# Kernel tuning notes

Measured on AMD Instinct MI355X. Metric: run time of the kernel, lower is better.

## Reference

```python
import jax, jax.numpy as jnp
import numpy as np

RESOLUTION = 2 ** 8  # 256
N_POINTS = 2 ** 21


def setup_inputs() -> dict:
    key = jax.random.key(0)
    k1, k2 = jax.random.split(key)
    inp = jax.random.uniform(k1, (N_POINTS, 3), dtype=jnp.float32)
    grid = jax.random.normal(k2, (RESOLUTION, RESOLUTION, RESOLUTION, 3), dtype=jnp.float32) * 0.01
    return {"input": inp, "feature_params": grid}


def reference(input, feature_params):
    R = feature_params.shape[0]
    scaled = input * (R - 1)
    lower = jnp.clip(jnp.floor(scaled).astype(jnp.int32), 0, R - 2)
    upper = jnp.clip(lower + 1, 0, R - 1)
    t = scaled - lower.astype(scaled.dtype)
    xl, yl, zl = lower[:, 0], lower[:, 1], lower[:, 2]
    xu, yu, zu = upper[:, 0], upper[:, 1], upper[:, 2]
    tx, ty, tz = t[:, 0:1], t[:, 1:2], t[:, 2:3]  # (N,1) for broadcast over channels
    # note original indexes grid as [z, y, x]
    c000 = feature_params[zl, yl, xl]
    c001 = feature_params[zl, yl, xu]
    c010 = feature_params[zl, yu, xl]
    c011 = feature_params[zl, yu, xu]
    c100 = feature_params[zu, yl, xl]
    c101 = feature_params[zu, yl, xu]
    c110 = feature_params[zu, yu, xl]
    c111 = feature_params[zu, yu, xu]
    c00 = c000 * (1 - tx) + c001 * tx
    c01 = c010 * (1 - tx) + c011 * tx
    c10 = c100 * (1 - tx) + c101 * tx
    c11 = c110 * (1 - tx) + c111 * tx
    c0 = c00 * (1 - ty) + c01 * ty
    c1 = c10 * (1 - ty) + c11 * ty
    return c0 * (1 - tz) + c1 * tz
```

## Files before the change

kernel.cpp:

```cpp
#include <hip/hip_runtime.h>


#define NB     8192
#define CAP    512u
#define GBLK   512
#define BPB    16
#define CHUNKF 100
#define NCHUNK 81
#define NF4    2025
#define LDSF   8100

#define CUR_OFF   67108864u
#define NEEDED    (67108864u + 32768u)

typedef float f4v __attribute__((ext_vector_type(4)));
typedef float f2v __attribute__((ext_vector_type(2)));
typedef f4v f4u __attribute__((aligned(8)));
typedef f2v f2u __attribute__((aligned(8)));

__device__ __forceinline__ void cell_of(float p, int& l, float& t) {
    float s = p * 255.0f;
    int v = (int)floorf(s);
    v = v < 0 ? 0 : (v > 254 ? 254 : v);
    l = v;
    t = s - (float)v;
}

__device__ __forceinline__ int fine_bin3(float px, float py, float pz) {
    int xl, yl, zl; float tx, ty, tz;
    cell_of(px, xl, tx);
    cell_of(py, yl, ty);
    cell_of(pz, zl, tz);
    return ((zl >> 3) << 8) | ((yl >> 3) << 3) | (xl >> 5);
}

__device__ __forceinline__ void direct_lerp(const float* __restrict__ grid,
                                            float* __restrict__ out, int i,
                                            int xl, int yl, int zl,
                                            float tx, float ty, float tz) {
    int b00 = (zl * 65536 + yl * 256 + xl) * 3;
    int b01 = b00 + 768, b10 = b00 + 196608, b11 = b10 + 768;
    float s00[6], s01[6], s10[6], s11[6];
#pragma unroll
    for (int k = 0; k < 6; ++k) s00[k] = grid[b00 + k];
#pragma unroll
    for (int k = 0; k < 6; ++k) s01[k] = grid[b01 + k];
#pragma unroll
    for (int k = 0; k < 6; ++k) s10[k] = grid[b10 + k];
#pragma unroll
    for (int k = 0; k < 6; ++k) s11[k] = grid[b11 + k];
#pragma unroll
    for (int c = 0; c < 3; ++c) {
        float c00 = s00[c] * (1.0f - tx) + s00[c + 3] * tx;
        float c01 = s01[c] * (1.0f - tx) + s01[c + 3] * tx;
        float c10 = s10[c] * (1.0f - tx) + s10[c + 3] * tx;
        float c11 = s11[c] * (1.0f - tx) + s11[c + 3] * tx;
        float c0 = c00 * (1.0f - ty) + c01 * ty;
        float c1 = c10 * (1.0f - ty) + c11 * ty;
        out[3 * i + c] = c0 * (1.0f - tz) + c1 * tz;
    }
}

__global__ __launch_bounds__(1024) void k_init(unsigned* __restrict__ cur) {
    int i = blockIdx.x * 1024 + threadIdx.x;
    if (i < NB) cur[i] = (unsigned)i * CAP;
}

__global__ __launch_bounds__(1024) void k_scatter(const float* __restrict__ inp,
                                                  const float* __restrict__ grid,
                                                  float4* __restrict__ binned,
                                                  unsigned* __restrict__ cur,
                                                  float* __restrict__ out, int n) {
    __shared__ unsigned cnt[NB];
    __shared__ unsigned base[NB];
    int t = threadIdx.x;
    int P = n >> 1;
    int stride = gridDim.x * 1024;
    int iters = (P + stride - 1) / stride;

    if ((n & 1) && blockIdx.x == 0 && t == 0) {
        int i = n - 1;
        float px = inp[3 * i], py = inp[3 * i + 1], pz = inp[3 * i + 2];
        int b = fine_bin3(px, py, pz);
        unsigned r = atomicAdd(&cur[b], 1u);
        if (r - (unsigned)b * CAP < CAP) {
            float4 v; v.x = px; v.y = py; v.z = pz; v.w = __uint_as_float((unsigned)i);
            binned[r] = v;
        } else {
            int xl, yl, zl; float tx, ty, tz;
            cell_of(px, xl, tx); cell_of(py, yl, ty); cell_of(pz, zl, tz);
            direct_lerp(grid, out, i, xl, yl, zl, tx, ty, tz);
        }
    }

    for (int it = 0; it < iters; ++it) {
        int pr = it * stride + blockIdx.x * 1024 + t;
        for (int k = t; k < NB; k += 1024) cnt[k] = 0;
        __syncthreads();
        int b0 = 0, b1 = 0; unsigned r0 = 0, r1 = 0;
        float4 p0, p1;
        bool valid = (pr < P);
        if (valid) {
            f4v a = *(const f4u*)(inp + 6 * pr);
            f2v b = *(const f2u*)(inp + 6 * pr + 4);
            p0.x = a.x; p0.y = a.y; p0.z = a.z;
            p0.w = __uint_as_float((unsigned)(2 * pr));
            p1.x = a.w; p1.y = b.x; p1.z = b.y;
            p1.w = __uint_as_float((unsigned)(2 * pr + 1));
            b0 = fine_bin3(p0.x, p0.y, p0.z);
            b1 = fine_bin3(p1.x, p1.y, p1.z);
            r0 = atomicAdd(&cnt[b0], 1u);
            r1 = atomicAdd(&cnt[b1], 1u);
        }
        __syncthreads();
        for (int k = t; k < NB; k += 1024)
            if (cnt[k]) base[k] = atomicAdd(&cur[k], cnt[k]);
        __syncthreads();
        if (valid) {
            unsigned s0 = base[b0] + r0;
            unsigned s1 = base[b1] + r1;
            if (s0 - (unsigned)b0 * CAP < CAP) binned[s0] = p0;
            else {
                int xl, yl, zl; float tx, ty, tz;
                cell_of(p0.x, xl, tx); cell_of(p0.y, yl, ty); cell_of(p0.z, zl, tz);
                direct_lerp(grid, out, 2 * pr, xl, yl, zl, tx, ty, tz);
            }
            if (s1 - (unsigned)b1 * CAP < CAP) binned[s1] = p1;
            else {
                int xl, yl, zl; float tx, ty, tz;
                cell_of(p1.x, xl, tx); cell_of(p1.y, yl, ty); cell_of(p1.z, zl, tz);
                direct_lerp(grid, out, 2 * pr + 1, xl, yl, zl, tx, ty, tz);
            }
        }
        __syncthreads();
    }
}

#define STAGE_SLAB(binv, dst)                                                   \
    do {                                                                        \
        int x0_ = ((binv) & 7) << 5;                                            \
        int y0_ = (((binv) >> 3) & 31) << 3;                                    \
        int z0_ = ((binv) >> 8) << 3;                                           \
        for (int u = t; u < NF4; u += GBLK) {                                   \
            int chunk = u / 25;                                                 \
            int j = u - chunk * 25;                                             \
            int zc = chunk / 9;                                                 \
            int yc = chunk - zc * 9;                                            \
            int zg = z0_ + zc; zg = zg > 255 ? 255 : zg;                        \
            int yg = y0_ + yc; yg = yg > 255 ? 255 : yg;                        \
            int joff = (j == 24 && x0_ == 224) ? 0 : (j << 2);                  \
            const float* src =                                                  \
                grid + (size_t)((zg << 16) | (yg << 8) | x0_) * 3 + joff;       \
            __builtin_amdgcn_global_load_lds(                                   \
                (const __attribute__((address_space(1))) unsigned int*)src,     \
                (__attribute__((address_space(3))) unsigned int*)&(dst)[(size_t)u * 4], \
                16, 0, 0);                                                      \
        }                                                                       \
    } while (0)

__global__ __launch_bounds__(GBLK) void k_gather(const float4* __restrict__ binned,
                                                 const float* __restrict__ grid,
                                                 const unsigned* __restrict__ cur,
                                                 float* __restrict__ out) {
    __shared__ __align__(16) float slab[2][LDSF];
    int t = threadIdx.x;
    int sb = ((blockIdx.x & 7) << 6) | (blockIdx.x >> 3);
    int bin0 = sb * BPB;

    STAGE_SLAB(bin0, slab[0]);

    for (int k = 0; k < BPB; ++k) {
        int bin = bin0 + k;
        int cb = k & 1;
        __syncthreads();
        if (k + 1 < BPB) STAGE_SLAB(bin + 1, slab[cb ^ 1]);

        int x0 = (bin & 7) << 5;
        int y0 = ((bin >> 3) & 31) << 3;
        int z0 = (bin >> 8) << 3;
        unsigned start = (unsigned)bin * CAP;
        unsigned count = cur[bin] - start;
        if (count > CAP) count = CAP;

        for (unsigned p = (unsigned)t; p < count; p += (unsigned)GBLK) {
            float4 v = binned[start + p];
            unsigned idx = __float_as_uint(v.w);

            int xl, yl, zl; float tx, ty, tz;
            cell_of(v.x, xl, tx);
            cell_of(v.y, yl, ty);
            cell_of(v.z, zl, tz);
            int xc = xl - x0, yc = yl - y0, zc = zl - z0;

            int r0 = (zc * 9 + yc) * CHUNKF + xc * 3;
            int e = r0 & ~1;
            bool d = (r0 & 1) != 0;

#define SEG_READ(b, s)                                       \
            do {                                             \
                f2v q0 = *(const f2u*)(&slab[cb][(b)]);      \
                f2v q1 = *(const f2u*)(&slab[cb][(b) + 2]);  \
                f2v q2 = *(const f2u*)(&slab[cb][(b) + 4]);  \
                f2v q3 = *(const f2u*)(&slab[cb][(b) + 6]);  \
                s[0] = d ? q0.y : q0.x;                      \
                s[1] = d ? q1.x : q0.y;                      \
                s[2] = d ? q1.y : q1.x;                      \
                s[3] = d ? q2.x : q1.y;                      \
                s[4] = d ? q2.y : q2.x;                      \
                s[5] = d ? q3.x : q2.y;                      \
            } while (0)

            float s00[6], s01[6], s10[6], s11[6];
            SEG_READ(e,               s00);
            SEG_READ(e + CHUNKF,      s01);
            SEG_READ(e + 9 * CHUNKF,  s10);
            SEG_READ(e + 10 * CHUNKF, s11);
#undef SEG_READ

            float o[3];
#pragma unroll
            for (int c = 0; c < 3; ++c) {
                float c00 = s00[c] * (1.0f - tx) + s00[c + 3] * tx;
                float c01 = s01[c] * (1.0f - tx) + s01[c + 3] * tx;
                float c10 = s10[c] * (1.0f - tx) + s10[c + 3] * tx;
                float c11 = s11[c] * (1.0f - tx) + s11[c + 3] * tx;
                float c0 = c00 * (1.0f - ty) + c01 * ty;
                float c1 = c10 * (1.0f - ty) + c11 * ty;
                o[c] = c0 * (1.0f - tz) + c1 * tz;
            }
            float3 w; w.x = o[0]; w.y = o[1]; w.z = o[2];
            *(float3*)(out + 3 * (size_t)idx) = w;
        }
    }
}

__global__ __launch_bounds__(256) void k_direct(const float* __restrict__ inp,
                                                const float* __restrict__ grid,
                                                float* __restrict__ out, int n) {
    int i = blockIdx.x * blockDim.x + threadIdx.x;
    if (i >= n) return;
    int xl, yl, zl; float tx, ty, tz;
    cell_of(inp[3 * i + 0], xl, tx);
    cell_of(inp[3 * i + 1], yl, ty);
    cell_of(inp[3 * i + 2], zl, tz);
    direct_lerp(grid, out, i, xl, yl, zl, tx, ty, tz);
}

extern "C" void kernel_launch(void* const* d_in, const int* in_sizes, int n_in,
                              void* d_out, int out_size, void* d_ws, size_t ws_size,
                              hipStream_t stream) {
    const float* inp  = (const float*)d_in[0];
    const float* grid = (const float*)d_in[1];
    float* out = (float*)d_out;
    int n = in_sizes[0] / 3;

    if (ws_size < (size_t)NEEDED) {
        int blocks = (n + 255) / 256;
        k_direct<<<blocks, 256, 0, stream>>>(inp, grid, out, n);
        return;
    }

    char* ws = (char*)d_ws;
    float4*   binned = (float4*)ws;
    unsigned* cur    = (unsigned*)(ws + CUR_OFF);

    k_init   <<<8,        1024, 0, stream>>>(cur);
    k_scatter<<<512,      1024, 0, stream>>>(inp, grid, binned, cur, out, n);
    k_gather <<<NB / BPB, GBLK, 0, stream>>>(binned, grid, cur, out);
}
```

Measured before the change: 143.9 us.

## Rebin points into z-layer × y-band bins and stream grid layers through a 3-slot LDS ring

Bins become one z-layer by an 8-row y-band across the full x width, replacing 32x8x8 bricks. Each gather block walks 16 consecutive z-layers and keeps a triple-buffered ring of grid layers in LDS. Each staged layer serves two consecutive z bins, which cuts redundant halo loads, and the staging copies contiguous memory instead of strided chunks. Blocks grow to 1024 threads and the grid shrinks to 512 blocks. The risks are lower occupancy from the larger LDS footprint and fewer, bigger blocks.

```diff
diff --git a/kernel.cpp b/kernel.cpp
--- a/kernel.cpp
+++ b/kernel.cpp
@@ -3,12 +3,10 @@
 
 #define NB     8192
 #define CAP    512u
-#define GBLK   512
-#define BPB    16
-#define CHUNKF 100
-#define NCHUNK 81
-#define NF4    2025
-#define LDSF   8100
+#define GBLK   1024
+#define LAYERF4 1728
+#define LAYERF  6912
+#define GRIDF4  12582912
 
 #define CUR_OFF   67108864u
 #define NEEDED    (67108864u + 32768u)
@@ -31,7 +29,7 @@
     cell_of(px, xl, tx);
     cell_of(py, yl, ty);
     cell_of(pz, zl, tz);
-    return ((zl >> 3) << 8) | ((yl >> 3) << 3) | (xl >> 5);
+    return (zl << 5) | (yl >> 3);
 }
 
 __device__ __forceinline__ void direct_lerp(const float* __restrict__ grid,
@@ -136,24 +134,16 @@
     }
 }
 
-#define STAGE_SLAB(binv, dst)                                                   \
+#define STAGE_LAYER(zg_, slot_)                                                 \
     do {                                                                        \
-        int x0_ = ((binv) & 7) << 5;                                            \
-        int y0_ = (((binv) >> 3) & 31) << 3;                                    \
-        int z0_ = ((binv) >> 8) << 3;                                           \
-        for (int u = t; u < NF4; u += GBLK) {                                   \
-            int chunk = u / 25;                                                 \
-            int j = u - chunk * 25;                                             \
-            int zc = chunk / 9;                                                 \
-            int yc = chunk - zc * 9;                                            \
-            int zg = z0_ + zc; zg = zg > 255 ? 255 : zg;                        \
-            int yg = y0_ + yc; yg = yg > 255 ? 255 : yg;                        \
-            int joff = (j == 24 && x0_ == 224) ? 0 : (j << 2);                  \
-            const float* src =                                                  \
-                grid + (size_t)((zg << 16) | (yg << 8) | x0_) * 3 + joff;       \
+        size_t basef4 = (size_t)(zg_)*49152 + (size_t)y0 * 192;                 \
+        float* dst = &slab[(slot_) * LAYERF];                                   \
+        for (int u = t; u < LAYERF4; u += GBLK) {                               \
+            size_t sf4 = basef4 + (size_t)u;                                    \
+            if (sf4 > (size_t)(GRIDF4 - 1)) sf4 = (size_t)(GRIDF4 - 1);         \
             __builtin_amdgcn_global_load_lds(                                   \
-                (const __attribute__((address_space(1))) unsigned int*)src,     \
-                (__attribute__((address_space(3))) unsigned int*)&(dst)[(size_t)u * 4], \
+                (const __attribute__((address_space(1))) unsigned int*)(grid + sf4 * 4), \
+                (__attribute__((address_space(3))) unsigned int*)&dst[(size_t)u * 4], \
                 16, 0, 0);                                                      \
         }                                                                       \
     } while (0)
@@ -162,24 +152,30 @@
                                                  const float* __restrict__ grid,
                                                  const unsigned* __restrict__ cur,
                                                  float* __restrict__ out) {
-    __shared__ __align__(16) float slab[2][LDSF];
+    __shared__ __align__(16) float slab[3 * LAYERF];
     int t = threadIdx.x;
-    int sb = ((blockIdx.x & 7) << 6) | (blockIdx.x >> 3);
-    int bin0 = sb * BPB;
-
-    STAGE_SLAB(bin0, slab[0]);
-
-    for (int k = 0; k < BPB; ++k) {
-        int bin = bin0 + k;
-        int cb = k & 1;
-        __syncthreads();
-        if (k + 1 < BPB) STAGE_SLAB(bin + 1, slab[cb ^ 1]);
-
-        int x0 = (bin & 7) << 5;
-        int y0 = ((bin >> 3) & 31) << 3;
-        int z0 = (bin >> 8) << 3;
-        unsigned start = (unsigned)bin * CAP;
-        unsigned count = cur[bin] - start;
+    int bin = ((blockIdx.x & 7) << 6) | (blockIdx.x >> 3);
+    int zb = bin >> 5;
+    int yb = bin & 31;
+    int z0 = zb << 4;
+    int y0 = yb << 3;
+
+    int zg1 = z0 + 1 > 255 ? 255 : z0 + 1;
+    STAGE_LAYER(z0,  0);
+    STAGE_LAYER(zg1, 1);
+
+    for (int zc = 0; zc < 16; ++zc) {
+        int sA = (zc % 3) * LAYERF;
+        int sB = ((zc + 1) % 3) * LAYERF;
+        __syncthreads();
+        if (zc < 15) {
+            int zg = z0 + zc + 2; zg = zg > 255 ? 255 : zg;
+            STAGE_LAYER(zg, (zc + 2) % 3);
+        }
+
+        int K = ((z0 + zc) << 5) | yb;
+        unsigned start = (unsigned)K * CAP;
+        unsigned count = cur[K] - start;
         if (count > CAP) count = CAP;
 
         for (unsigned p = (unsigned)t; p < count; p += (unsigned)GBLK) {
@@ -190,31 +186,34 @@
             cell_of(v.x, xl, tx);
             cell_of(v.y, yl, ty);
             cell_of(v.z, zl, tz);
-            int xc = xl - x0, yc = yl - y0, zc = zl - z0;
-
-            int r0 = (zc * 9 + yc) * CHUNKF + xc * 3;
-            int e = r0 & ~1;
-            bool d = (r0 & 1) != 0;
-
-#define SEG_READ(b, s)                                       \
-            do {                                             \
-                f2v q0 = *(const f2u*)(&slab[cb][(b)]);      \
-                f2v q1 = *(const f2u*)(&slab[cb][(b) + 2]);  \
-                f2v q2 = *(const f2u*)(&slab[cb][(b) + 4]);  \
-                f2v q3 = *(const f2u*)(&slab[cb][(b) + 6]);  \
-                s[0] = d ? q0.y : q0.x;                      \
-                s[1] = d ? q1.x : q0.y;                      \
-                s[2] = d ? q1.y : q1.x;                      \
-                s[3] = d ? q2.x : q1.y;                      \
-                s[4] = d ? q2.y : q2.x;                      \
-                s[5] = d ? q3.x : q2.y;                      \
+            int row = yl - y0;
+
+            int o00 = sA + row * 768 + xl * 3;
+            int o01 = o00 + 768;
+            int o10 = sB + row * 768 + xl * 3;
+            int o11 = o10 + 768;
+
+#define SEG_READ(b, s)                                   \
+            do {                                         \
+                int e_ = (b) & ~1;                       \
+                bool d_ = ((b) & 1) != 0;                \
+                f2v q0 = *(const f2u*)(&slab[e_]);       \
+                f2v q1 = *(const f2u*)(&slab[e_ + 2]);   \
+                f2v q2 = *(const f2u*)(&slab[e_ + 4]);   \
+                f2v q3 = *(const f2u*)(&slab[e_ + 6]);   \
+                s[0] = d_ ? q0.y : q0.x;                 \
+                s[1] = d_ ? q1.x : q0.y;                 \
+                s[2] = d_ ? q1.y : q1.x;                 \
+                s[3] = d_ ? q2.x : q1.y;                 \
+                s[4] = d_ ? q2.y : q2.x;                 \
+                s[5] = d_ ? q3.x : q2.y;                 \
             } while (0)
 
             float s00[6], s01[6], s10[6], s11[6];
-            SEG_READ(e,               s00);
-            SEG_READ(e + CHUNKF,      s01);
-            SEG_READ(e + 9 * CHUNKF,  s10);
-            SEG_READ(e + 10 * CHUNKF, s11);
+            SEG_READ(o00, s00);
+            SEG_READ(o01, s01);
+            SEG_READ(o10, s10);
+            SEG_READ(o11, s11);
 #undef SEG_READ
 
             float o[3];
@@ -264,7 +263,7 @@
     float4*   binned = (float4*)ws;
     unsigned* cur    = (unsigned*)(ws + CUR_OFF);
 
-    k_init   <<<8,        1024, 0, stream>>>(cur);
-    k_scatter<<<512,      1024, 0, stream>>>(inp, grid, binned, cur, out, n);
-    k_gather <<<NB / BPB, GBLK, 0, stream>>>(binned, grid, cur, out);
-}
+    k_init   <<<8,   1024, 0, stream>>>(cur);
+    k_scatter<<<512, 1024, 0, stream>>>(inp, grid, binned, cur, out, n);
+    k_gather <<<512, GBLK, 0, stream>>>(binned, grid, cur, out);
+}
```

After: 136.8 us. -4.9%, faster.
